# Kernel tuning notes

Hardware: AMD Instinct MI355X
Metric: run time of the kernel (lower is better)

## Reference

```python
import jax, jax.numpy as jnp
import numpy as np

T, B, E, H = 128, 1024, 1024, 1024  # batch must equal hidden (original code uses Whh @ h)


def setup_inputs() -> dict:
    key = jax.random.key(0)
    ks = jax.random.split(key, 10)
    s = 1.0 / np.sqrt(H).astype(np.float32)  # ~xavier scale, avoids gate saturation
    inp = {
        'X': jax.random.normal(ks[0], (T, B, E), dtype=jnp.float32),
        'Wii': jax.random.normal(ks[1], (E, H), dtype=jnp.float32) * s,
        'Whi': jax.random.normal(ks[2], (H, H), dtype=jnp.float32) * s,
        'bi': jnp.zeros((H,), dtype=jnp.float32),
        'Wif': jax.random.normal(ks[3], (E, H), dtype=jnp.float32) * s,
        'Whf': jax.random.normal(ks[4], (H, H), dtype=jnp.float32) * s,
        'bf': jnp.zeros((H,), dtype=jnp.float32),
        'Wig': jax.random.normal(ks[5], (E, H), dtype=jnp.float32) * s,
        'Whg': jax.random.normal(ks[6], (H, H), dtype=jnp.float32) * s,
        'bg': jnp.zeros((H,), dtype=jnp.float32),
        'Wio': jax.random.normal(ks[7], (E, H), dtype=jnp.float32) * s,
        'Who': jax.random.normal(ks[8], (H, H), dtype=jnp.float32) * s,
        'bo': jnp.zeros((H,), dtype=jnp.float32),
    }
    return inp


def reference(X, Wii, Whi, bi, Wif, Whf, bf, Wig, Whg, bg, Wio, Who, bo):
    # Faithful to the original: recurrent term is Whh @ h (NOT h @ Whh),
    # which requires batch == hidden as in the source module.
    batch = X.shape[1]
    hid = Wii.shape[1]
    h0 = jnp.zeros((batch, hid), dtype=X.dtype)
    c0 = jnp.zeros((batch, hid), dtype=X.dtype)

    def step(carry, x_t):
        h, c = carry
        i = jax.nn.sigmoid(x_t @ Wii + Whi @ h + bi)
        f = jax.nn.sigmoid(x_t @ Wif + Whf @ h + bf)
        g = jnp.tanh(x_t @ Wig + Whg @ h + bg)
        o = jax.nn.sigmoid(x_t @ Wio + Who @ h + bo)
        c_new = f * c + i * g
        h_new = o * jnp.tanh(c_new)
        return (h_new, c_new), h_new

    (h_t, c_t), hidden_sequence = jax.lax.scan(step, (h0, c0), X)
    return hidden_sequence, (h_t, c_t)
```

## Files before the change

kernel.cpp:

```cpp
#include <hip/hip_runtime.h>
#include <cstdint>

typedef __attribute__((ext_vector_type(8))) short bf16x8;
typedef __attribute__((ext_vector_type(4))) float f32x4;
typedef __attribute__((ext_vector_type(4))) unsigned int u32x4;

#define AS1 __attribute__((address_space(1)))
#define AS3 __attribute__((address_space(3)))

__device__ __forceinline__ unsigned short f2bf(float f) {
  unsigned int u = __builtin_bit_cast(unsigned int, f);
  return (unsigned short)((u + 0x7fffu + ((u >> 16) & 1u)) >> 16);
}
__device__ __forceinline__ float bf2f(unsigned short h) {
  unsigned int u = ((unsigned int)h) << 16;
  return __builtin_bit_cast(float, u);
}
__device__ __forceinline__ float sigm(float x) { return 1.f / (1.f + __expf(-x)); }
__device__ __forceinline__ float tanh_f(float x) {
  float e = __expf(2.f * x);
  return 1.f - 2.f / (e + 1.f);
}
__device__ __forceinline__ void gload16(const void* g, void* l) {
  __builtin_amdgcn_global_load_lds((const AS1 unsigned int*)g, (AS3 unsigned int*)l, 16, 0, 0);
}
__device__ __forceinline__ int swz(int e) { return e ^ (((e >> 6) & 7) << 3); }


__global__ __launch_bounds__(256) void conv_wh_kernel(
    const float4* __restrict__ w0, const float4* __restrict__ w1,
    const float4* __restrict__ w2, const float4* __restrict__ w3,
    unsigned long long* __restrict__ dst) {
  int i = blockIdx.x * 256 + threadIdx.x;
  int g = i >> 18;
  const float4* s = g == 0 ? w0 : g == 1 ? w1 : g == 2 ? w2 : w3;
  float4 v = s[i & 0x3FFFF];
  unsigned long long p = (unsigned long long)f2bf(v.x) |
                         ((unsigned long long)f2bf(v.y) << 16) |
                         ((unsigned long long)f2bf(v.z) << 32) |
                         ((unsigned long long)f2bf(v.w) << 48);
  dst[i] = p;
}

__global__ __launch_bounds__(256) void conv_wiT_kernel(
    const float* __restrict__ w0, const float* __restrict__ w1,
    const float* __restrict__ w2, const float* __restrict__ w3,
    unsigned short* __restrict__ dst) {
  __shared__ unsigned short ls[64][72];
  int bid = blockIdx.x;
  int g = bid >> 8;
  int t2 = bid & 255;
  int tj = t2 & 15, tk = t2 >> 4;
  const float* W = g == 0 ? w0 : g == 1 ? w1 : g == 2 ? w2 : w3;
  int k0 = tk * 64, j0 = tj * 64;
  int ty = threadIdx.x >> 6, tx = threadIdx.x & 63;
#pragma unroll
  for (int r = 0; r < 16; ++r) {
    int k = k0 + ty * 16 + r;
    ls[tx][ty * 16 + r] = f2bf(W[k * 1024 + j0 + tx]);
  }
  __syncthreads();
#pragma unroll
  for (int r = 0; r < 16; ++r) {
    int jl = ty * 16 + r;
    dst[(size_t)(g * 1024 + j0 + jl) * 1024 + k0 + tx] = ls[jl][tx];
  }
}

__global__ __launch_bounds__(256) void conv_bias_kernel(
    const float* __restrict__ b0, const float* __restrict__ b1,
    const float* __restrict__ b2, const float* __restrict__ b3,
    float* __restrict__ dst) {
  int i = blockIdx.x * 256 + threadIdx.x;
  const float* s = (i >> 10) == 0 ? b0 : (i >> 10) == 1 ? b1 : (i >> 10) == 2 ? b2 : b3;
  dst[i] = s[i & 1023];
}

__global__ __launch_bounds__(256) void conv_x_kernel(
    const float4* __restrict__ src, unsigned long long* __restrict__ dst, int n4) {
  int i = blockIdx.x * 256 + threadIdx.x;
  if (i < n4) {
    float4 v = src[i];
    dst[i] = (unsigned long long)f2bf(v.x) |
             ((unsigned long long)f2bf(v.y) << 16) |
             ((unsigned long long)f2bf(v.z) << 32) |
             ((unsigned long long)f2bf(v.w) << 48);
  }
}

__global__ __launch_bounds__(512) void xproj_gemm_kernel(
    const unsigned short* __restrict__ A,
    const unsigned short* __restrict__ Bt,
    unsigned short* __restrict__ C,
    int Mc) {
  __shared__ __align__(16) unsigned short smem[2][2][256 * 64];
  int xcd = blockIdx.x & 7;
  int i5 = blockIdx.x >> 3;
  int bn = xcd * 2 + (i5 & 1);
  int bm = i5 >> 1;
  int m0 = bm * 256, n0 = bn * 256;
  int tid = threadIdx.x, w = tid >> 6, lane = tid & 63;
  int wm = w >> 2, wn = w & 3;
  int l15 = lane & 15, l4 = lane >> 4;

  f32x4 acc[8][4];
#pragma unroll
  for (int i = 0; i < 8; ++i)
#pragma unroll
    for (int j = 0; j < 4; ++j) acc[i][j] = (f32x4)0.f;

  auto stageHalf = [&](int buf, int kt, int X) {
    int kk = kt * 64;
    unsigned short* dst = &smem[buf][X & 1][0];
    const unsigned short* src = (X & 1) ? Bt : A;
    int gbase = (X & 1) ? n0 : m0;
    int r0 = (X >> 1) * 128;
#pragma unroll
    for (int u = 0; u < 2; ++u) {
      int cid = u * 512 + tid;
      int rl = r0 + (cid >> 3), s = cid & 7;
      int sk = kk + ((s ^ (rl & 7)) << 3);
      gload16(&src[(size_t)(gbase + rl) * 1024 + sk],
              &dst[r0 * 64 + (u * 512 + w * 64) * 8]);
    }
  };
  auto rdA = [&](int buf, int lo, bf16x8 (&arr)[4][2]) {
#pragma unroll
    for (int mf = 0; mf < 4; ++mf)
#pragma unroll
      for (int kss = 0; kss < 2; ++kss) {
        int row = lo * 128 + wm * 64 + mf * 16 + l15;
        arr[mf][kss] =
            *(const bf16x8*)&smem[buf][0][swz(row * 64 + kss * 32 + l4 * 8)];
      }
  };
  auto rdB = [&](int buf, int lo, bf16x8 (&arr)[2][2]) {
#pragma unroll
    for (int nf = 0; nf < 2; ++nf)
#pragma unroll
      for (int kss = 0; kss < 2; ++kss) {
        int row = lo * 128 + wn * 32 + nf * 16 + l15;
        arr[nf][kss] =
            *(const bf16x8*)&smem[buf][1][swz(row * 64 + kss * 32 + l4 * 8)];
      }
  };

  bf16x8 af03[4][2], af47[4][2], bfr01[2][2], bfr23[2][2];

  auto cl1 = [&] {
#pragma unroll
    for (int mf = 0; mf < 4; ++mf)
#pragma unroll
      for (int nf = 0; nf < 2; ++nf)
#pragma unroll
        for (int k = 0; k < 2; ++k)
          acc[mf][nf] = __builtin_amdgcn_mfma_f32_16x16x32_bf16(
              af03[mf][k], bfr01[nf][k], acc[mf][nf], 0, 0, 0);
  };
  auto cl2 = [&] {
#pragma unroll
    for (int mf = 0; mf < 4; ++mf)
#pragma unroll
      for (int nf = 0; nf < 2; ++nf)
#pragma unroll
        for (int k = 0; k < 2; ++k)
          acc[4 + mf][nf] = __builtin_amdgcn_mfma_f32_16x16x32_bf16(
              af47[mf][k], bfr01[nf][k], acc[4 + mf][nf], 0, 0, 0);
  };
  auto cl3 = [&] {
#pragma unroll
    for (int mf = 0; mf < 4; ++mf)
#pragma unroll
      for (int nf = 0; nf < 2; ++nf)
#pragma unroll
        for (int k = 0; k < 2; ++k)
          acc[mf][2 + nf] = __builtin_amdgcn_mfma_f32_16x16x32_bf16(
              af03[mf][k], bfr23[nf][k], acc[mf][2 + nf], 0, 0, 0);
  };
  auto cl4 = [&] {
#pragma unroll
    for (int mf = 0; mf < 4; ++mf)
#pragma unroll
      for (int nf = 0; nf < 2; ++nf)
#pragma unroll
        for (int k = 0; k < 2; ++k)
          acc[4 + mf][2 + nf] = __builtin_amdgcn_mfma_f32_16x16x32_bf16(
              af47[mf][k], bfr23[nf][k], acc[4 + mf][2 + nf], 0, 0, 0);
  };

  stageHalf(0, 0, 0); stageHalf(0, 0, 1); stageHalf(0, 0, 2); stageHalf(0, 0, 3);
  asm volatile("s_waitcnt vmcnt(6)" ::: "memory");
  __builtin_amdgcn_sched_barrier(0);
  __builtin_amdgcn_s_barrier();
  __builtin_amdgcn_sched_barrier(0);

  for (int t = 0; t < 16; ++t) {
    int c = t & 1;
    rdA(c, 0, af03);
    if (t + 1 < 16) stageHalf(c ^ 1, t + 1, 0);
    if (t < 15) asm volatile("s_waitcnt vmcnt(6)" ::: "memory");
    else        asm volatile("s_waitcnt vmcnt(4)" ::: "memory");
    __builtin_amdgcn_sched_barrier(0);
    __builtin_amdgcn_s_barrier();
    __builtin_amdgcn_sched_barrier(0);
    asm volatile("s_waitcnt lgkmcnt(0)" ::: "memory");
    __builtin_amdgcn_sched_barrier(0);
    if (t > 0) {
      __builtin_amdgcn_s_setprio(1);
      cl4();
      __builtin_amdgcn_s_setprio(0);
    }
    rdB(c, 0, bfr01);
    if (t + 1 < 16) stageHalf(c ^ 1, t + 1, 1);
    if (t < 15) asm volatile("s_waitcnt vmcnt(6)" ::: "memory");
    else        asm volatile("s_waitcnt vmcnt(2)" ::: "memory");
    __builtin_amdgcn_sched_barrier(0);
    __builtin_amdgcn_s_barrier();
    __builtin_amdgcn_sched_barrier(0);
    asm volatile("s_waitcnt lgkmcnt(0)" ::: "memory");
    __builtin_amdgcn_sched_barrier(0);
    __builtin_amdgcn_s_setprio(1);
    cl1();
    __builtin_amdgcn_s_setprio(0);
    rdA(c, 1, af47);
    if (t + 1 < 16) stageHalf(c ^ 1, t + 1, 2);
    if (t < 15) asm volatile("s_waitcnt vmcnt(6)" ::: "memory");
    else        asm volatile("s_waitcnt vmcnt(0)" ::: "memory");
    __builtin_amdgcn_sched_barrier(0);
    __builtin_amdgcn_s_barrier();
    __builtin_amdgcn_sched_barrier(0);
    asm volatile("s_waitcnt lgkmcnt(0)" ::: "memory");
    __builtin_amdgcn_sched_barrier(0);
    __builtin_amdgcn_s_setprio(1);
    cl2();
    __builtin_amdgcn_s_setprio(0);
    rdB(c, 1, bfr23);
    if (t + 1 < 16) stageHalf(c ^ 1, t + 1, 3);
    if (t < 15) asm volatile("s_waitcnt vmcnt(6)" ::: "memory");
    else        asm volatile("s_waitcnt vmcnt(0)" ::: "memory");
    __builtin_amdgcn_sched_barrier(0);
    __builtin_amdgcn_s_barrier();
    __builtin_amdgcn_sched_barrier(0);
    asm volatile("s_waitcnt lgkmcnt(0)" ::: "memory");
    __builtin_amdgcn_sched_barrier(0);
    __builtin_amdgcn_s_setprio(1);
    cl3();
    __builtin_amdgcn_s_setprio(0);
  }
  __builtin_amdgcn_s_setprio(1);
  cl4();
  __builtin_amdgcn_s_setprio(0);

  unsigned short* lsC = &smem[0][0][0];
#pragma unroll
  for (int h = 0; h < 2; ++h) {
    __syncthreads();
#pragma unroll
    for (int mf = 0; mf < 8; ++mf)
#pragma unroll
      for (int f = 0; f < 2; ++f) {
        int nf = h * 2 + f;
        int rowl = (mf < 4 ? wm * 64 + mf * 16 : 128 + wm * 64 + (mf - 4) * 16)
                   + l4 * 4;
        int coll = wn * 32 + f * 16 + l15;
#pragma unroll
        for (int r = 0; r < 4; ++r)
          lsC[(rowl + r) * 136 + coll] = f2bf(acc[mf][nf][r]);
      }
    __syncthreads();
#pragma unroll
    for (int u = 0; u < 8; ++u) {
      int chunk = u * 512 + tid;
      int row = chunk >> 4, c8 = chunk & 15;
      u32x4 v = *(const u32x4*)&lsC[row * 136 + c8 * 8];
      __builtin_nontemporal_store(
          v, (u32x4*)&C[(size_t)(m0 + row) * 4096 + n0 + h * 128 + c8 * 8]);
    }
  }
}

__global__ __launch_bounds__(256) void lstm_step_kernel(
    const unsigned short* __restrict__ Wh,
    const unsigned short* __restrict__ hT,
    const unsigned short* __restrict__ Xp,
    const float* __restrict__ bias,
    float* __restrict__ cst,
    float* __restrict__ out_h,
    float* __restrict__ out_ht,
    float* __restrict__ out_ct,
    unsigned short* __restrict__ hT_next,
    int isLast) {
  __shared__ unsigned short lsA[3][128 * 64];
  __shared__ unsigned short lsB[3][64 * 64];
  int bx = blockIdx.x;
  int xcd = bx & 7, idx = bx >> 3;
  int bb = xcd * 4 + (idx & 3);
  int bj = idx >> 2;
  int b0 = bb * 32, j0 = bj * 64;
  int tid = threadIdx.x, w = tid >> 6, lane = tid & 63;
  int wm = w >> 1, wn = w & 1;
  int l15 = lane & 15, l4 = lane >> 4;
  int bbase = b0 + wm * 16 + l4 * 4;

  float bias_pre[4][2];
  float c_pre[2][4];
  unsigned short xp_pre[4][2][4];
#pragma unroll
  for (int n = 0; n < 2; ++n) {
    int j = j0 + wn * 32 + n * 16 + l15;
#pragma unroll
    for (int g = 0; g < 4; ++g) bias_pre[g][n] = bias[g * 1024 + j];
#pragma unroll
    for (int r = 0; r < 4; ++r) {
      c_pre[n][r] = cst[(size_t)(bbase + r) * 1024 + j];
#pragma unroll
      for (int g = 0; g < 4; ++g)
        xp_pre[g][n][r] = Xp[(size_t)(bbase + r) * 4096 + g * 1024 + j];
    }
  }

  f32x4 acc[4][2];
#pragma unroll
  for (int g = 0; g < 4; ++g)
#pragma unroll
    for (int n = 0; n < 2; ++n) acc[g][n] = (f32x4)0.f;

  auto stage = [&](int buf, int kk) {
#pragma unroll
    for (int ld = 0; ld < 4; ++ld) {
      int cid = ld * 256 + tid;
      int r = cid >> 3, kc = (cid & 7) * 8;
      int sk = kk + (kc ^ ((r & 7) << 3));
      int grow = ((r >> 4) & 3) * 1024 + b0 + (r >> 6) * 16 + (r & 15);
      gload16(&Wh[(size_t)grow * 1024 + sk], &lsA[buf][(ld * 256 + w * 64) * 8]);
    }
#pragma unroll
    for (int u = 0; u < 2; ++u) {
      int cid = u * 256 + tid;
      int r = cid >> 3, kc = (cid & 7) * 8;
      int sk = kk + (kc ^ ((r & 7) << 3));
      gload16(&hT[(size_t)(j0 + r) * 1024 + sk], &lsB[buf][(u * 256 + w * 64) * 8]);
    }
  };
  auto compute = [&](int buf) {
    bf16x8 af[4][2], bfr[2][2];
#pragma unroll
    for (int g = 0; g < 4; ++g)
#pragma unroll
      for (int kss = 0; kss < 2; ++kss) {
        int e = (wm * 64 + g * 16 + l15) * 64 + kss * 32 + l4 * 8;
        af[g][kss] = *(const bf16x8*)&lsA[buf][swz(e)];
      }
#pragma unroll
    for (int n = 0; n < 2; ++n)
#pragma unroll
      for (int kss = 0; kss < 2; ++kss) {
        int e = (wn * 32 + n * 16 + l15) * 64 + kss * 32 + l4 * 8;
        bfr[n][kss] = *(const bf16x8*)&lsB[buf][swz(e)];
      }
    __builtin_amdgcn_s_setprio(1);
#pragma unroll
    for (int g = 0; g < 4; ++g)
#pragma unroll
      for (int n = 0; n < 2; ++n)
#pragma unroll
        for (int kss = 0; kss < 2; ++kss)
          acc[g][n] = __builtin_amdgcn_mfma_f32_16x16x32_bf16(
              af[g][kss], bfr[n][kss], acc[g][n], 0, 0, 0);
    __builtin_amdgcn_s_setprio(0);
  };

  stage(0, 0);
  stage(1, 64);
#pragma unroll
  for (int it = 0; it < 16; ++it) {
    if (it < 15) asm volatile("s_waitcnt vmcnt(6)" ::: "memory");
    else         asm volatile("s_waitcnt vmcnt(0)" ::: "memory");
    __builtin_amdgcn_sched_barrier(0);
    __builtin_amdgcn_s_barrier();
    __builtin_amdgcn_sched_barrier(0);
    if (it + 2 < 16) stage((it + 2) % 3, (it + 2) * 64);
    compute(it % 3);
    asm volatile("s_waitcnt lgkmcnt(0)" ::: "memory");
    __builtin_amdgcn_sched_barrier(0);
  }

#pragma unroll
  for (int n = 0; n < 2; ++n) {
    int j = j0 + wn * 32 + n * 16 + l15;
    float hn[4], cn[4];
#pragma unroll
    for (int r = 0; r < 4; ++r) {
      int b = bbase + r;
      float pi = acc[0][n][r] + bf2f(xp_pre[0][n][r]) + bias_pre[0][n];
      float pf = acc[1][n][r] + bf2f(xp_pre[1][n][r]) + bias_pre[1][n];
      float pg = acc[2][n][r] + bf2f(xp_pre[2][n][r]) + bias_pre[2][n];
      float po = acc[3][n][r] + bf2f(xp_pre[3][n][r]) + bias_pre[3][n];
      float ig = sigm(pi), fg = sigm(pf), gg = tanh_f(pg), og = sigm(po);
      float c_new = fg * c_pre[n][r] + ig * gg;
      cst[(size_t)b * 1024 + j] = c_new;
      cn[r] = c_new;
      hn[r] = og * tanh_f(c_new);
      __builtin_nontemporal_store(hn[r], &out_h[(size_t)b * 1024 + j]);
    }
    unsigned long long hp = (unsigned long long)f2bf(hn[0]) |
                            ((unsigned long long)f2bf(hn[1]) << 16) |
                            ((unsigned long long)f2bf(hn[2]) << 32) |
                            ((unsigned long long)f2bf(hn[3]) << 48);
    *(unsigned long long*)&hT_next[(size_t)j * 1024 + bbase] = hp;
    if (isLast) {
#pragma unroll
      for (int r = 0; r < 4; ++r) {
        int b = bbase + r;
        __builtin_nontemporal_store(hn[r], &out_ht[(size_t)b * 1024 + j]);
        __builtin_nontemporal_store(cn[r], &out_ct[(size_t)b * 1024 + j]);
      }
    }
  }
}

extern "C" void kernel_launch(void* const* d_in, const int* in_sizes, int n_in,
                              void* d_out, int out_size, void* d_ws, size_t ws_size,
                              hipStream_t stream) {
  const float* X   = (const float*)d_in[0];
  const float* Wii = (const float*)d_in[1];
  const float* Whi = (const float*)d_in[2];
  const float* bi  = (const float*)d_in[3];
  const float* Wif = (const float*)d_in[4];
  const float* Whf = (const float*)d_in[5];
  const float* bfv = (const float*)d_in[6];
  const float* Wig = (const float*)d_in[7];
  const float* Whg = (const float*)d_in[8];
  const float* bg  = (const float*)d_in[9];
  const float* Wio = (const float*)d_in[10];
  const float* Who = (const float*)d_in[11];
  const float* bo  = (const float*)d_in[12];
  float* out = (float*)d_out;

  char* wsp = (char*)d_ws;
  size_t off = 0;
  auto walloc = [&](size_t b) -> void* {
    void* p = wsp + off;
    off += (b + 255) & ~(size_t)255;
    return p;
  };
  unsigned short* WiT = (unsigned short*)walloc(4096ull * 1024 * 2);
  unsigned short* Wh  = (unsigned short*)walloc(4096ull * 1024 * 2);
  float* bias = (float*)walloc(4096 * 4);
  unsigned short* hT0 = (unsigned short*)walloc(1024ull * 1024 * 2);
  unsigned short* hT1 = (unsigned short*)walloc(1024ull * 1024 * 2);
  float* cbuf = (float*)walloc(1024ull * 1024 * 4);
  size_t fixed = off;

  long long avail = (long long)ws_size - (long long)fixed - (1ll << 20);
  int Tc = (int)(avail / (10ll << 20));
  if (Tc < 1) Tc = 1;
  if (Tc > 128) Tc = 128;
  unsigned short* Xbf = (unsigned short*)walloc((size_t)Tc * 1024 * 1024 * 2);
  unsigned short* Xp  = (unsigned short*)walloc((size_t)Tc * 1024 * 4096 * 2);

  conv_wh_kernel<<<4096, 256, 0, stream>>>((const float4*)Whi, (const float4*)Whf,
                                           (const float4*)Whg, (const float4*)Who,
                                           (unsigned long long*)Wh);
  conv_wiT_kernel<<<1024, 256, 0, stream>>>(Wii, Wif, Wig, Wio, WiT);
  conv_bias_kernel<<<16, 256, 0, stream>>>(bi, bfv, bg, bo, bias);
  hipMemsetAsync(hT0, 0, 1024ull * 1024 * 2, stream);
  hipMemsetAsync(cbuf, 0, 1024ull * 1024 * 4, stream);

  for (int t0 = 0; t0 < 128; t0 += Tc) {
    int tc = (128 - t0 < Tc) ? (128 - t0) : Tc;
    int n4 = tc * 262144;
    conv_x_kernel<<<n4 / 256, 256, 0, stream>>>(
        (const float4*)(X + (size_t)t0 * 1048576),
        (unsigned long long*)Xbf, n4);
    xproj_gemm_kernel<<<tc * 64, 512, 0, stream>>>(Xbf, WiT, Xp, tc * 1024);
    for (int i = 0; i < tc; ++i) {
      int t = t0 + i;
      lstm_step_kernel<<<512, 256, 0, stream>>>(
          Wh, (t & 1) ? hT1 : hT0,
          Xp + (size_t)i * 1024 * 4096,
          bias, cbuf,
          out + (size_t)t * 1048576,
          out + 134217728ull,
          out + 135266304ull,
          (t & 1) ? hT0 : hT1,
          (t == 127) ? 1 : 0);
    }
  }
}
```

Baseline: 3.366 ms.

## Shrink LSTM step tiles to 16x64 with K=32 stages and double the grid

```diff
diff --git a/kernel.cpp b/kernel.cpp
--- a/kernel.cpp
+++ b/kernel.cpp
@@ -25,6 +25,9 @@
   __builtin_amdgcn_global_load_lds((const AS1 unsigned int*)g, (AS3 unsigned int*)l, 16, 0, 0);
 }
 __device__ __forceinline__ int swz(int e) { return e ^ (((e >> 6) & 7) << 3); }
+__device__ __forceinline__ int sl32(int row, int slot) {
+  return row * 32 + ((slot ^ ((row >> 1) & 3)) << 3);
+}
 
 
 __global__ __launch_bounds__(256) void conv_wh_kernel(
@@ -279,142 +282,112 @@
   }
 }
 
-__global__ __launch_bounds__(256) void lstm_step_kernel(
+__global__ __launch_bounds__(256, 4) void lstm_step_kernel(
     const unsigned short* __restrict__ Wh,
     const unsigned short* __restrict__ hT,
     const unsigned short* __restrict__ Xp,
     const float* __restrict__ bias,
     float* __restrict__ cst,
-    float* __restrict__ out_h,
-    float* __restrict__ out_ht,
+    float* __restrict__ out_h, float* __restrict__ out_ht,
     float* __restrict__ out_ct,
     unsigned short* __restrict__ hT_next,
     int isLast) {
-  __shared__ unsigned short lsA[3][128 * 64];
-  __shared__ unsigned short lsB[3][64 * 64];
+  __shared__ unsigned short lsA[3][64 * 32];
+  __shared__ unsigned short lsB[3][64 * 32];
   int bx = blockIdx.x;
   int xcd = bx & 7, idx = bx >> 3;
-  int bb = xcd * 4 + (idx & 3);
-  int bj = idx >> 2;
-  int b0 = bb * 32, j0 = bj * 64;
+  int bb = xcd * 8 + (idx & 7);
+  int bj = idx >> 3;
+  int b0 = bb * 16, j0 = bj * 64;
   int tid = threadIdx.x, w = tid >> 6, lane = tid & 63;
-  int wm = w >> 1, wn = w & 1;
   int l15 = lane & 15, l4 = lane >> 4;
-  int bbase = b0 + wm * 16 + l4 * 4;
-
-  float bias_pre[4][2];
-  float c_pre[2][4];
-  unsigned short xp_pre[4][2][4];
-#pragma unroll
-  for (int n = 0; n < 2; ++n) {
-    int j = j0 + wn * 32 + n * 16 + l15;
-#pragma unroll
-    for (int g = 0; g < 4; ++g) bias_pre[g][n] = bias[g * 1024 + j];
-#pragma unroll
-    for (int r = 0; r < 4; ++r) {
-      c_pre[n][r] = cst[(size_t)(bbase + r) * 1024 + j];
-#pragma unroll
-      for (int g = 0; g < 4; ++g)
-        xp_pre[g][n][r] = Xp[(size_t)(bbase + r) * 4096 + g * 1024 + j];
-    }
-  }
-
-  f32x4 acc[4][2];
-#pragma unroll
-  for (int g = 0; g < 4; ++g)
-#pragma unroll
-    for (int n = 0; n < 2; ++n) acc[g][n] = (f32x4)0.f;
+  int bbase = b0 + l4 * 4;
+  int j = j0 + w * 16 + l15;
+
+  float bias_pre[4];
+  float c_pre[4];
+  unsigned short xp_pre[4][4];
+#pragma unroll
+  for (int g = 0; g < 4; ++g) bias_pre[g] = bias[g * 1024 + j];
+#pragma unroll
+  for (int r = 0; r < 4; ++r) {
+    c_pre[r] = cst[(size_t)(bbase + r) * 1024 + j];
+#pragma unroll
+    for (int g = 0; g < 4; ++g)
+      xp_pre[g][r] = Xp[(size_t)(bbase + r) * 4096 + g * 1024 + j];
+  }
+
+  f32x4 acc[4];
+#pragma unroll
+  for (int g = 0; g < 4; ++g) acc[g] = (f32x4)0.f;
 
   auto stage = [&](int buf, int kk) {
-#pragma unroll
-    for (int ld = 0; ld < 4; ++ld) {
-      int cid = ld * 256 + tid;
-      int r = cid >> 3, kc = (cid & 7) * 8;
-      int sk = kk + (kc ^ ((r & 7) << 3));
-      int grow = ((r >> 4) & 3) * 1024 + b0 + (r >> 6) * 16 + (r & 15);
-      gload16(&Wh[(size_t)grow * 1024 + sk], &lsA[buf][(ld * 256 + w * 64) * 8]);
-    }
-#pragma unroll
-    for (int u = 0; u < 2; ++u) {
-      int cid = u * 256 + tid;
-      int r = cid >> 3, kc = (cid & 7) * 8;
-      int sk = kk + (kc ^ ((r & 7) << 3));
-      gload16(&hT[(size_t)(j0 + r) * 1024 + sk], &lsB[buf][(u * 256 + w * 64) * 8]);
+    {
+      int r = tid >> 2, s = tid & 3;
+      int sk = kk + ((s ^ ((r >> 1) & 3)) << 3);
+      int grow = (r >> 4) * 1024 + b0 + (r & 15);
+      gload16(&Wh[(size_t)grow * 1024 + sk], &lsA[buf][tid * 8]);
+    }
+    {
+      int r = tid >> 2, s = tid & 3;
+      int sk = kk + ((s ^ ((r >> 1) & 3)) << 3);
+      gload16(&hT[(size_t)(j0 + r) * 1024 + sk], &lsB[buf][tid * 8]);
     }
   };
   auto compute = [&](int buf) {
-    bf16x8 af[4][2], bfr[2][2];
+    bf16x8 af[4], bfr;
 #pragma unroll
     for (int g = 0; g < 4; ++g)
-#pragma unroll
-      for (int kss = 0; kss < 2; ++kss) {
-        int e = (wm * 64 + g * 16 + l15) * 64 + kss * 32 + l4 * 8;
-        af[g][kss] = *(const bf16x8*)&lsA[buf][swz(e)];
-      }
-#pragma unroll
-    for (int n = 0; n < 2; ++n)
-#pragma unroll
-      for (int kss = 0; kss < 2; ++kss) {
-        int e = (wn * 32 + n * 16 + l15) * 64 + kss * 32 + l4 * 8;
-        bfr[n][kss] = *(const bf16x8*)&lsB[buf][swz(e)];
-      }
+      af[g] = *(const bf16x8*)&lsA[buf][sl32(g * 16 + l15, l4)];
+    bfr = *(const bf16x8*)&lsB[buf][sl32(w * 16 + l15, l4)];
     __builtin_amdgcn_s_setprio(1);
 #pragma unroll
     for (int g = 0; g < 4; ++g)
-#pragma unroll
-      for (int n = 0; n < 2; ++n)
-#pragma unroll
-        for (int kss = 0; kss < 2; ++kss)
-          acc[g][n] = __builtin_amdgcn_mfma_f32_16x16x32_bf16(
-              af[g][kss], bfr[n][kss], acc[g][n], 0, 0, 0);
+      acc[g] = __builtin_amdgcn_mfma_f32_16x16x32_bf16(af[g], bfr, acc[g], 0, 0, 0);
     __builtin_amdgcn_s_setprio(0);
   };
 
   stage(0, 0);
-  stage(1, 64);
-#pragma unroll
-  for (int it = 0; it < 16; ++it) {
-    if (it < 15) asm volatile("s_waitcnt vmcnt(6)" ::: "memory");
+  stage(1, 32);
+#pragma unroll
+  for (int it = 0; it < 32; ++it) {
+    if (it < 31) asm volatile("s_waitcnt vmcnt(2)" ::: "memory");
     else         asm volatile("s_waitcnt vmcnt(0)" ::: "memory");
     __builtin_amdgcn_sched_barrier(0);
     __builtin_amdgcn_s_barrier();
     __builtin_amdgcn_sched_barrier(0);
-    if (it + 2 < 16) stage((it + 2) % 3, (it + 2) * 64);
+    if (it + 2 < 32) stage((it + 2) % 3, (it + 2) * 32);
     compute(it % 3);
     asm volatile("s_waitcnt lgkmcnt(0)" ::: "memory");
     __builtin_amdgcn_sched_barrier(0);
   }
 
-#pragma unroll
-  for (int n = 0; n < 2; ++n) {
-    int j = j0 + wn * 32 + n * 16 + l15;
-    float hn[4], cn[4];
+  float hn[4], cn[4];
+#pragma unroll
+  for (int r = 0; r < 4; ++r) {
+    int b = bbase + r;
+    float pi = acc[0][r] + bf2f(xp_pre[0][r]) + bias_pre[0];
+    float pf = acc[1][r] + bf2f(xp_pre[1][r]) + bias_pre[1];
+    float pg = acc[2][r] + bf2f(xp_pre[2][r]) + bias_pre[2];
+    float po = acc[3][r] + bf2f(xp_pre[3][r]) + bias_pre[3];
+    float ig = sigm(pi), fg = sigm(pf), gg = tanh_f(pg), og = sigm(po);
+    float c_new = fg * c_pre[r] + ig * gg;
+    cst[(size_t)b * 1024 + j] = c_new;
+    cn[r] = c_new;
+    hn[r] = og * tanh_f(c_new);
+    __builtin_nontemporal_store(hn[r], &out_h[(size_t)b * 1024 + j]);
+  }
+  unsigned long long hp = (unsigned long long)f2bf(hn[0]) |
+                          ((unsigned long long)f2bf(hn[1]) << 16) |
+                          ((unsigned long long)f2bf(hn[2]) << 32) |
+                          ((unsigned long long)f2bf(hn[3]) << 48);
+  *(unsigned long long*)&hT_next[(size_t)j * 1024 + bbase] = hp;
+  if (isLast) {
 #pragma unroll
     for (int r = 0; r < 4; ++r) {
       int b = bbase + r;
-      float pi = acc[0][n][r] + bf2f(xp_pre[0][n][r]) + bias_pre[0][n];
-      float pf = acc[1][n][r] + bf2f(xp_pre[1][n][r]) + bias_pre[1][n];
-      float pg = acc[2][n][r] + bf2f(xp_pre[2][n][r]) + bias_pre[2][n];
-      float po = acc[3][n][r] + bf2f(xp_pre[3][n][r]) + bias_pre[3][n];
-      float ig = sigm(pi), fg = sigm(pf), gg = tanh_f(pg), og = sigm(po);
-      float c_new = fg * c_pre[n][r] + ig * gg;
-      cst[(size_t)b * 1024 + j] = c_new;
-      cn[r] = c_new;
-      hn[r] = og * tanh_f(c_new);
-      __builtin_nontemporal_store(hn[r], &out_h[(size_t)b * 1024 + j]);
-    }
-    unsigned long long hp = (unsigned long long)f2bf(hn[0]) |
-                            ((unsigned long long)f2bf(hn[1]) << 16) |
-                            ((unsigned long long)f2bf(hn[2]) << 32) |
-                            ((unsigned long long)f2bf(hn[3]) << 48);
-    *(unsigned long long*)&hT_next[(size_t)j * 1024 + bbase] = hp;
-    if (isLast) {
-#pragma unroll
-      for (int r = 0; r < 4; ++r) {
-        int b = bbase + r;
-        __builtin_nontemporal_store(hn[r], &out_ht[(size_t)b * 1024 + j]);
-        __builtin_nontemporal_store(cn[r], &out_ct[(size_t)b * 1024 + j]);
-      }
+      __builtin_nontemporal_store(hn[r], &out_ht[(size_t)b * 1024 + j]);
+      __builtin_nontemporal_store(cn[r], &out_ct[(size_t)b * 1024 + j]);
     }
   }
 }
@@ -476,7 +449,7 @@
     xproj_gemm_kernel<<<tc * 64, 512, 0, stream>>>(Xbf, WiT, Xp, tc * 1024);
     for (int i = 0; i < tc; ++i) {
       int t = t0 + i;
-      lstm_step_kernel<<<512, 256, 0, stream>>>(
+      lstm_step_kernel<<<1024, 256, 0, stream>>>(
           Wh, (t & 1) ? hT1 : hT0,
           Xp + (size_t)i * 1024 * 4096,
           bias, cbuf,
```

Measured after the change: 3.890 ms. +15.6%, slower.
